# Kernel optimization log

Hardware: AMD Instinct MI355X
Metric: run time of the kernel (lower is better)

## Reference

```python
import jax, jax.numpy as jnp
import numpy as np

DIM = 2048
N_HEADS = 16
N_KV_HEADS = 4
HEAD_DIM = DIM // N_HEADS  # 128
N_REP = N_HEADS // N_KV_HEADS  # 4
SEQ = 2048
BATCH = 2


def apply_rope(x, cos, sin):
    # x: [b, s, h, d]; cos/sin: [s, d//2]
    xr = x[..., 0::2]
    xi = x[..., 1::2]
    c = cos[None, :, None, :]
    s = sin[None, :, None, :]
    out_r = xr * c - xi * s
    out_i = xr * s + xi * c
    # interleave back: stack on last axis then flatten
    out = jnp.stack([out_r, out_i], axis=-1)
    return out.reshape(x.shape)


def setup_inputs() -> dict:
    key = jax.random.key(0)
    ks = jax.random.split(key, 7)
    x = jax.random.normal(ks[0], (BATCH, SEQ, DIM), dtype=jnp.float32)
    # realistic rotary tables
    inv_freq = 1.0 / (10000.0 ** (np.arange(0, HEAD_DIM, 2, dtype=np.float32) / HEAD_DIM))
    t = np.arange(SEQ, dtype=np.float32)
    freqs = np.outer(t, inv_freq)  # [S, d//2]
    freqs_cos = jnp.asarray(np.cos(freqs))
    freqs_sin = jnp.asarray(np.sin(freqs))
    sc = 0.02
    Wq = jax.random.normal(ks[1], (DIM, N_HEADS * HEAD_DIM), dtype=jnp.float32) * sc
    Wk = jax.random.normal(ks[2], (DIM, N_KV_HEADS * HEAD_DIM), dtype=jnp.float32) * sc
    Wv = jax.random.normal(ks[3], (DIM, N_KV_HEADS * HEAD_DIM), dtype=jnp.float32) * sc
    Wo = jax.random.normal(ks[4], (N_HEADS * HEAD_DIM, DIM), dtype=jnp.float32) * sc
    return {"x": x, "freqs_cos": freqs_cos, "freqs_sin": freqs_sin,
            "Wq": Wq, "Wk": Wk, "Wv": Wv, "Wo": Wo}


def reference(x, freqs_cos, freqs_sin, Wq, Wk, Wv, Wo):
    b, s, _ = x.shape
    xq = (x @ Wq).reshape(b, s, N_HEADS, HEAD_DIM)
    xk = (x @ Wk).reshape(b, s, N_KV_HEADS, HEAD_DIM)
    xv = (x @ Wv).reshape(b, s, N_KV_HEADS, HEAD_DIM)
    xq = apply_rope(xq, freqs_cos, freqs_sin)
    xk = apply_rope(xk, freqs_cos, freqs_sin)
    # GQA attention without materializing repeated KV:
    # group query heads as [b, g, r, s, d] with g=N_KV_HEADS, r=N_REP
    q = xq.reshape(b, s, N_KV_HEADS, N_REP, HEAD_DIM)
    scale = 1.0 / jnp.sqrt(jnp.float32(HEAD_DIM))
    scores = jnp.einsum('bqgrd,bkgd->bgrqk', q, xk) * scale  # [b,g,r,s,s]
    causal = jnp.tril(jnp.ones((s, s), dtype=bool))
    scores = jnp.where(causal[None, None, None], scores, jnp.finfo(scores.dtype).min)
    probs = jax.nn.softmax(scores, axis=-1)
    out = jnp.einsum('bgrqk,bkgd->bqgrd', probs, xv)  # [b,s,g,r,d]
    out = out.reshape(b, s, N_HEADS * HEAD_DIM)
    return out @ Wo
```

## Files before the change

kernel.cpp:

```cpp
#include <hip/hip_runtime.h>
#include <stdint.h>
#include <stddef.h>

constexpr int BATCH = 2;
constexpr int SEQ   = 2048;
constexpr int EMB   = 2048;
constexpr int HEADS = 16;
constexpr int GQA   = 4;
constexpr int HDIM  = 128;
constexpr int NQKV  = 3072;
constexpr int VOFF  = 2560;
constexpr int MROWS = BATCH * SEQ;

typedef _Float16 half8  __attribute__((ext_vector_type(8)));
typedef _Float16 half4v __attribute__((ext_vector_type(4)));
typedef float    floatx4 __attribute__((ext_vector_type(4)));

__device__ __forceinline__ void st_c(float* p, float v)    { *p = v; }
__device__ __forceinline__ void st_c(_Float16* p, float v) { *p = (_Float16)v; }

__device__ __forceinline__ void gld16(const _Float16* g, _Float16* l) {
    __builtin_amdgcn_global_load_lds(
        (const __attribute__((address_space(1))) void*)g,
        (__attribute__((address_space(3))) void*)l, 16, 0, 0);
}

__global__ void cast_x_kernel(const float* __restrict__ x, _Float16* __restrict__ xh) {
    int i = (blockIdx.x * 256 + threadIdx.x) * 4;
    float4 v = *(const float4*)(x + i);
    half4v h;
    h[0] = (_Float16)v.x; h[1] = (_Float16)v.y; h[2] = (_Float16)v.z; h[3] = (_Float16)v.w;
    *(half4v*)(xh + i) = h;
}

__global__ void transpose_cast(const float* __restrict__ in, _Float16* __restrict__ out,
                               int R, int C) {
    __shared__ float tile[32][33];
    int cb = blockIdx.x * 32, rb = blockIdx.y * 32;
    int tx = threadIdx.x, ty = threadIdx.y;
    #pragma unroll
    for (int j = 0; j < 32; j += 8)
        tile[ty + j][tx] = in[(size_t)(rb + ty + j) * C + (cb + tx)];
    __syncthreads();
    #pragma unroll
    for (int j = 0; j < 32; j += 8)
        out[(size_t)(cb + ty + j) * R + (rb + tx)] = (_Float16)tile[tx][ty + j];
}

__global__ void transpose_cast_qkv(const float* __restrict__ Wq, const float* __restrict__ Wk,
                                   const float* __restrict__ Wv, _Float16* __restrict__ out) {
    __shared__ float tile[32][33];
    int cb = blockIdx.x * 32, rb = blockIdx.y * 32;
    const float* src; int C, cl;
    if (cb < 2048)      { src = Wq; C = 2048; cl = cb; }
    else if (cb < 2560) { src = Wk; C = 512;  cl = cb - 2048; }
    else                { src = Wv; C = 512;  cl = cb - 2560; }
    int tx = threadIdx.x, ty = threadIdx.y;
    #pragma unroll
    for (int j = 0; j < 32; j += 8)
        tile[ty + j][tx] = src[(size_t)(rb + ty + j) * C + (cl + tx)];
    __syncthreads();
    #pragma unroll
    for (int j = 0; j < 32; j += 8)
        out[(size_t)(cb + ty + j) * EMB + (rb + tx)] = (_Float16)tile[tx][ty + j];
}

template <typename CT, bool ROPE, int RXW, int RYH>
__global__ __launch_bounds__(256) void gemm_bt(const _Float16* __restrict__ A,
                                               const _Float16* __restrict__ Bt,
                                               CT* __restrict__ C,
                                               int M, int N, int K,
                                               const float* __restrict__ fc,
                                               const float* __restrict__ fs) {
    __shared__ _Float16 As[2][128 * 32];
    __shared__ _Float16 Bs[2][128 * 32];
    const int tid  = threadIdx.x;
    const int bid = blockIdx.y * (2 * RXW) + blockIdx.x;
    const int xcd = bid & 7, loc = bid >> 3;
    const int bxi = (xcd & 1) * RXW + (loc % RXW);
    const int byi = (xcd >> 1) * RYH + (loc / RXW);
    const int bm  = byi * 128, bn = bxi * 128;
    const int lane = tid & 63, wid = tid >> 6;
    const int wr   = wid >> 1, wc = wid & 1;
    const int qd   = lane >> 4, m15 = lane & 15;

    const int srow = lane >> 2;
    const int scol = (lane & 3) * 8;
    const _Float16* Ag = A  + (size_t)(bm + wid * 16 + srow) * K + scol;
    const _Float16* Bg = Bt + (size_t)(bn + wid * 16 + srow) * K + scol;
    const size_t rowskip = (size_t)64 * K;
    const int woff = wid * 16 * 32;

    gld16(Ag,           &As[0][woff]);
    gld16(Ag + rowskip, &As[0][woff + 64 * 32]);
    gld16(Bg,           &Bs[0][woff]);
    gld16(Bg + rowskip, &Bs[0][woff + 64 * 32]);

    floatx4 acc[4][4] = {};
    const int nk = K >> 5;

    for (int kt = 0; kt < nk; ++kt) {
        const int cur = kt & 1;
        __syncthreads();
        if (kt + 1 < nk) {
            const int ko = (kt + 1) * 32;
            _Float16* aw = &As[cur ^ 1][woff];
            _Float16* bw = &Bs[cur ^ 1][woff];
            gld16(Ag + ko,           aw);
            gld16(Ag + rowskip + ko, aw + 64 * 32);
            gld16(Bg + ko,           bw);
            gld16(Bg + rowskip + ko, bw + 64 * 32);
        }
        const _Float16* AsR = &As[cur][(wr * 64 + m15) * 32 + qd * 8];
        const _Float16* BsR = &Bs[cur][(wc * 64 + m15) * 32 + qd * 8];
        half8 af[4], bf[4];
        #pragma unroll
        for (int i = 0; i < 4; i++) af[i] = *(const half8*)(AsR + i * 16 * 32);
        #pragma unroll
        for (int i = 0; i < 4; i++) bf[i] = *(const half8*)(BsR + i * 16 * 32);
        #pragma unroll
        for (int mi = 0; mi < 4; mi++)
            #pragma unroll
            for (int ni = 0; ni < 4; ni++)
                acc[mi][ni] = __builtin_amdgcn_mfma_f32_16x16x32_f16(af[mi], bf[ni], acc[mi][ni], 0, 0, 0);
    }

    #pragma unroll
    for (int mi = 0; mi < 4; mi++)
        #pragma unroll
        for (int ni = 0; ni < 4; ni++)
            #pragma unroll
            for (int r = 0; r < 4; r++) {
                int row = bm + wr * 64 + mi * 16 + qd * 4 + r;
                int col = bn + wc * 64 + ni * 16 + m15;
                float v = acc[mi][ni][r];
                if (ROPE && col < VOFF) {
                    int si = row & (SEQ - 1);
                    int fi = (col >> 1) & 63;
                    float c  = fc[si * 64 + fi];
                    float sn = fs[si * 64 + fi];
                    float other = __shfl_xor(v, 1, 64);
                    v = (m15 & 1) ? (v * c + other * sn) : (v * c - other * sn);
                }
                st_c(&C[(size_t)row * N + col], v);
            }
}

__global__ void transpose_v(const _Float16* __restrict__ qkv, _Float16* __restrict__ vt) {
    __shared__ _Float16 tile[32][33];
    int sb = blockIdx.x * 32, db = blockIdx.y * 32;
    int bg = blockIdx.z;
    int tx = threadIdx.x, ty = threadIdx.y;
    const _Float16* src = qkv + (size_t)(bg >> 2) * SEQ * NQKV + VOFF + (bg & 3) * HDIM;
    #pragma unroll
    for (int j = 0; j < 32; j += 8)
        tile[ty + j][tx] = src[(size_t)(sb + ty + j) * NQKV + db + tx];
    __syncthreads();
    _Float16* dst = vt + (size_t)bg * HDIM * SEQ;
    #pragma unroll
    for (int j = 0; j < 32; j += 8)
        dst[(size_t)(db + ty + j) * SEQ + sb + tx] = tile[tx][ty + j];
}

__global__ __launch_bounds__(512, 2) void flash_attn(const _Float16* __restrict__ qkv,
                                                     const _Float16* __restrict__ vt,
                                                     _Float16* __restrict__ ob) {
    const int bx   = blockIdx.x;
    const int g    = blockIdx.y;
    const int b    = blockIdx.z;
    const int tid  = threadIdx.x;
    const int lane = tid & 63, wid = tid >> 6;
    const int h    = g * 4 + (wid & 3);
    const int su   = wid >> 2;
    const int qd   = lane >> 4, m15 = lane & 15;

    __shared__ _Float16 Ks[2][64 * 128];
    __shared__ _Float16 Vs[2][128 * 64];
    __shared__ _Float16 Ps[8][16 * 64];

    const _Float16* kg = qkv + (size_t)(b * SEQ) * NQKV + EMB + g * HDIM;
    const _Float16* vg = vt + (size_t)(b * GQA + g) * HDIM * SEQ;
    _Float16* pw = Ps[wid];

    const int kl = lane >> 4, kc16 = lane & 15;
    const int vl = lane >> 3, vc8  = lane & 7;
    const _Float16* kgp[2]; const _Float16* vgp[2];
    int ksoff[2], vsoff[2];
    #pragma unroll
    for (int j = 0; j < 2; j++) {
        int t = wid * 2 + j;
        int kr = t * 4 + kl;
        kgp[j] = kg + (size_t)kr * NQKV + ((kc16 ^ (kr & 15)) * 8);
        ksoff[j] = t * 512;
        int vr = t * 8 + vl;
        vgp[j] = vg + (size_t)vr * SEQ + ((vc8 ^ (vr & 7)) * 8);
        vsoff[j] = t * 512;
    }

    half8 ones;
    #pragma unroll
    for (int i = 0; i < 8; i++) ones[i] = (_Float16)1.0f;
    const _Float16 qsc = (_Float16)(0.08838834764831845f * 1.44269504088896341f);

    for (int ph = 0; ph < 2; ++ph) {
        const int sidx   = ph ? bx : 63 - bx;
        const int q0     = sidx * 32;
        const int ktLast = sidx >> 1;

        __syncthreads();
        #pragma unroll
        for (int j = 0; j < 2; j++) gld16(kgp[j], &Ks[0][ksoff[j]]);
        #pragma unroll
        for (int j = 0; j < 2; j++) gld16(vgp[j], &Vs[0][vsoff[j]]);

        half8 qf[4];
        {
            const _Float16* qb = qkv + (size_t)(b * SEQ + q0 + su * 16 + m15) * NQKV + h * HDIM + qd * 8;
            #pragma unroll
            for (int kc = 0; kc < 4; kc++) {
                half8 q = *(const half8*)(qb + kc * 32);
                #pragma unroll
                for (int i = 0; i < 8; i++) q[i] = (_Float16)(q[i] * qsc);
                qf[kc] = q;
            }
        }

        floatx4 o[9] = {};

        for (int kt = 0; kt <= ktLast; ++kt) {
            const int cur = kt & 1;
            __syncthreads();
            if (kt < ktLast) {
                const int nb = cur ^ 1;
                const size_t ko = (size_t)(kt + 1) * 64;
                #pragma unroll
                for (int j = 0; j < 2; j++) gld16(kgp[j] + ko * NQKV, &Ks[nb][ksoff[j]]);
                #pragma unroll
                for (int j = 0; j < 2; j++) gld16(vgp[j] + ko, &Vs[nb][vsoff[j]]);
            }
            const _Float16* ksb = Ks[cur];
            const _Float16* vsb = Vs[cur];

            floatx4 sa[4] = {};
            __builtin_amdgcn_s_setprio(1);
            #pragma unroll
            for (int nt = 0; nt < 4; ++nt) {
                const int kr = nt * 16 + m15;
                #pragma unroll
                for (int kc = 0; kc < 4; ++kc) {
                    half8 kf = *(const half8*)(&ksb[kr * 128 + (((kc * 4 + qd) ^ (kr & 15)) * 8)]);
                    sa[nt] = __builtin_amdgcn_mfma_f32_16x16x32_f16(qf[kc], kf, sa[nt], 0, 0, 0);
                }
            }
            __builtin_amdgcn_s_setprio(0);

            const bool diag = (kt == ktLast);
            const int  k0   = kt * 64;
            #pragma unroll
            for (int r = 0; r < 4; r++) {
                const int prow = qd * 4 + r;
                const int rowg = q0 + su * 16 + prow;
                #pragma unroll
                for (int nt = 0; nt < 4; nt++) {
                    float p = __builtin_exp2f(sa[nt][r]);
                    if (diag && (k0 + nt * 16 + m15 > rowg)) p = 0.f;
                    int chunk = (nt * 2 + (m15 >> 3)) ^ (prow & 7);
                    pw[prow * 64 + chunk * 8 + (m15 & 7)] = (_Float16)p;
                }
            }

            half8 pf[2];
            #pragma unroll
            for (int kc = 0; kc < 2; kc++)
                pf[kc] = *(const half8*)(&pw[m15 * 64 + (((kc * 4 + qd) ^ (m15 & 7)) * 8)]);

            __builtin_amdgcn_s_setprio(1);
            #pragma unroll
            for (int dt = 0; dt < 8; dt++) {
                const int vr = dt * 16 + m15;
                #pragma unroll
                for (int kc = 0; kc < 2; kc++) {
                    half8 vf = *(const half8*)(&vsb[vr * 64 + (((kc * 4 + qd) ^ (vr & 7)) * 8)]);
                    o[dt] = __builtin_amdgcn_mfma_f32_16x16x32_f16(pf[kc], vf, o[dt], 0, 0, 0);
                }
            }
            o[8] = __builtin_amdgcn_mfma_f32_16x16x32_f16(pf[0], ones, o[8], 0, 0, 0);
            o[8] = __builtin_amdgcn_mfma_f32_16x16x32_f16(pf[1], ones, o[8], 0, 0, 0);
            __builtin_amdgcn_s_setprio(0);
        }

        float linv[4];
        #pragma unroll
        for (int r = 0; r < 4; r++) linv[r] = 1.0f / o[8][r];
        _Float16* od = ob + (size_t)(b * SEQ + q0 + su * 16) * EMB + h * HDIM;
        #pragma unroll
        for (int dt = 0; dt < 8; dt++)
            #pragma unroll
            for (int r = 0; r < 4; r++)
                od[(size_t)(qd * 4 + r) * EMB + dt * 16 + m15] = (_Float16)(o[dt][r] * linv[r]);
    }
}

extern "C" void kernel_launch(void* const* d_in, const int* in_sizes, int n_in,
                              void* d_out, int out_size, void* d_ws, size_t ws_size,
                              hipStream_t stream) {
    (void)in_sizes; (void)n_in; (void)out_size; (void)ws_size;
    const float* x  = (const float*)d_in[0];
    const float* fc = (const float*)d_in[1];
    const float* fs = (const float*)d_in[2];
    const float* Wq = (const float*)d_in[3];
    const float* Wk = (const float*)d_in[4];
    const float* Wv = (const float*)d_in[5];
    const float* Wo = (const float*)d_in[6];
    float* out = (float*)d_out;

    _Float16* Xb   = (_Float16*)d_ws;
    _Float16* Wqkv = Xb   + (size_t)MROWS * EMB;
    _Float16* WoT  = Wqkv + (size_t)NQKV * EMB;
    _Float16* C1   = WoT  + (size_t)EMB * EMB;
    _Float16* Vt   = Wqkv;
    _Float16* Ob   = Xb;

    dim3 tb(32, 8);
    cast_x_kernel<<<MROWS * EMB / 1024, 256, 0, stream>>>(x, Xb);
    transpose_cast_qkv<<<dim3(NQKV / 32, EMB / 32), tb, 0, stream>>>(Wq, Wk, Wv, Wqkv);
    transpose_cast<<<dim3(EMB / 32, EMB / 32), tb, 0, stream>>>(Wo, WoT, EMB, EMB);

    gemm_bt<_Float16, true, 12, 8><<<dim3(NQKV / 128, MROWS / 128), 256, 0, stream>>>(
        Xb, Wqkv, C1, MROWS, NQKV, EMB, fc, fs);
    transpose_v<<<dim3(SEQ / 32, HDIM / 32, BATCH * GQA), tb, 0, stream>>>(C1, Vt);
    flash_attn<<<dim3(32, GQA, BATCH), 512, 0, stream>>>(C1, Vt, Ob);
    gemm_bt<float, false, 8, 8><<<dim3(EMB / 128, MROWS / 128), 256, 0, stream>>>(
        Ob, WoT, out, MROWS, EMB, EMB, nullptr, nullptr);
}
```

Baseline: 317.1 us.

## Double GEMM K-tile to 64 with XOR-swizzled LDS layout

The shared GEMM kernel now stages 128x64 tiles per K-step instead of 128x32, halving the number of barriers and loop iterations over K. The 16-byte chunks in LDS are XOR-swizzled by row so that MFMA fragment reads from the wider rows avoid bank conflicts. In exchange, LDS use doubles to 64 KB per block, which may lower occupancy, and each thread issues more global-to-LDS loads per step.

```diff
diff --git a/kernel.cpp b/kernel.cpp
--- a/kernel.cpp
+++ b/kernel.cpp
@@ -72,8 +72,8 @@
                                                int M, int N, int K,
                                                const float* __restrict__ fc,
                                                const float* __restrict__ fs) {
-    __shared__ _Float16 As[2][128 * 32];
-    __shared__ _Float16 Bs[2][128 * 32];
+    __shared__ _Float16 As[2][128 * 64];
+    __shared__ _Float16 Bs[2][128 * 64];
     const int tid  = threadIdx.x;
     const int bid = blockIdx.y * (2 * RXW) + blockIdx.x;
     const int xcd = bid & 7, loc = bid >> 3;
@@ -84,45 +84,52 @@
     const int wr   = wid >> 1, wc = wid & 1;
     const int qd   = lane >> 4, m15 = lane & 15;
 
-    const int srow = lane >> 2;
-    const int scol = (lane & 3) * 8;
-    const _Float16* Ag = A  + (size_t)(bm + wid * 16 + srow) * K + scol;
-    const _Float16* Bg = Bt + (size_t)(bn + wid * 16 + srow) * K + scol;
-    const size_t rowskip = (size_t)64 * K;
-    const int woff = wid * 16 * 32;
-
-    gld16(Ag,           &As[0][woff]);
-    gld16(Ag + rowskip, &As[0][woff + 64 * 32]);
-    gld16(Bg,           &Bs[0][woff]);
-    gld16(Bg + rowskip, &Bs[0][woff + 64 * 32]);
+    const int srow   = lane >> 3;
+    const int schunk = (lane & 7) ^ (srow & 7);
+    const _Float16* Ag = A  + (size_t)(bm + wid * 32 + srow) * K + schunk * 8;
+    const _Float16* Bg = Bt + (size_t)(bn + wid * 32 + srow) * K + schunk * 8;
+    const int woff = wid * 32 * 64;
 
     floatx4 acc[4][4] = {};
-    const int nk = K >> 5;
-
-    for (int kt = 0; kt < nk; ++kt) {
+    const int nt = K >> 6;
+
+    #pragma unroll
+    for (int j = 0; j < 4; j++) {
+        gld16(Ag + (size_t)(j * 8) * K, &As[0][woff + j * 8 * 64]);
+        gld16(Bg + (size_t)(j * 8) * K, &Bs[0][woff + j * 8 * 64]);
+    }
+
+    const int rs = m15 & 7;
+
+    for (int kt = 0; kt < nt; ++kt) {
         const int cur = kt & 1;
         __syncthreads();
-        if (kt + 1 < nk) {
-            const int ko = (kt + 1) * 32;
-            _Float16* aw = &As[cur ^ 1][woff];
-            _Float16* bw = &Bs[cur ^ 1][woff];
-            gld16(Ag + ko,           aw);
-            gld16(Ag + rowskip + ko, aw + 64 * 32);
-            gld16(Bg + ko,           bw);
-            gld16(Bg + rowskip + ko, bw + 64 * 32);
+        if (kt + 1 < nt) {
+            const int ko = (kt + 1) * 64;
+            #pragma unroll
+            for (int j = 0; j < 4; j++) {
+                gld16(Ag + (size_t)(j * 8) * K + ko, &As[cur ^ 1][woff + j * 8 * 64]);
+                gld16(Bg + (size_t)(j * 8) * K + ko, &Bs[cur ^ 1][woff + j * 8 * 64]);
+            }
         }
-        const _Float16* AsR = &As[cur][(wr * 64 + m15) * 32 + qd * 8];
-        const _Float16* BsR = &Bs[cur][(wc * 64 + m15) * 32 + qd * 8];
-        half8 af[4], bf[4];
-        #pragma unroll
-        for (int i = 0; i < 4; i++) af[i] = *(const half8*)(AsR + i * 16 * 32);
-        #pragma unroll
-        for (int i = 0; i < 4; i++) bf[i] = *(const half8*)(BsR + i * 16 * 32);
-        #pragma unroll
-        for (int mi = 0; mi < 4; mi++)
-            #pragma unroll
-            for (int ni = 0; ni < 4; ni++)
-                acc[mi][ni] = __builtin_amdgcn_mfma_f32_16x16x32_f16(af[mi], bf[ni], acc[mi][ni], 0, 0, 0);
+        const _Float16* Ab = As[cur];
+        const _Float16* Bb = Bs[cur];
+        #pragma unroll
+        for (int kk = 0; kk < 2; kk++) {
+            const int csw = ((kk * 4 + qd) ^ rs) * 8;
+            half8 af[4], bf[4];
+            #pragma unroll
+            for (int i = 0; i < 4; i++)
+                af[i] = *(const half8*)(Ab + (wr * 64 + i * 16 + m15) * 64 + csw);
+            #pragma unroll
+            for (int i = 0; i < 4; i++)
+                bf[i] = *(const half8*)(Bb + (wc * 64 + i * 16 + m15) * 64 + csw);
+            #pragma unroll
+            for (int mi = 0; mi < 4; mi++)
+                #pragma unroll
+                for (int ni = 0; ni < 4; ni++)
+                    acc[mi][ni] = __builtin_amdgcn_mfma_f32_16x16x32_f16(af[mi], bf[ni], acc[mi][ni], 0, 0, 0);
+        }
     }
 
     #pragma unroll
```

New measurement: 324.5 us. 2.4% more time.
